# Optimization experiments

Measured on AMD Instinct MI355X. Metric: run time of the kernel, lower is better.

## Reference

```python
import jax, jax.numpy as jnp
import numpy as np

# Dimensions (see shape_source)
D = 12       # tree depth / number of levels
N = 32768    # nodes per level
L = 3        # label_size
K = 4        # nary (max children)
HID = 128    # hidden_size == dim_E == dim_rep
V = 50000    # word_vocab_size
LAYERS = 2   # stacked NaryTreeLSTM layers


def setup_inputs() -> dict:
    key = jax.random.key(0)
    ks = jax.random.split(key, 10)
    s = 0.02  # weight init scale
    tokens = jax.random.randint(ks[0], (D, N, L), 0, V)
    # child indices in [-1, N]; -1 = no child, 0 = zero init row, 1..N = prev-level node
    indices = jax.random.randint(ks[1], (D, N, K), 0, N + 2) - 1
    E = jax.random.normal(ks[2], (V, HID))  # torch.randn init
    lin_w = jax.random.normal(ks[3], (HID, L * HID)) * s
    lin_b = jnp.zeros((HID,), jnp.float32)
    Uf_w = jax.random.normal(ks[4], (LAYERS, K * HID, K * HID)) * s
    Uf_b = jnp.zeros((LAYERS, K * HID), jnp.float32)
    Uiuo_w = jax.random.normal(ks[5], (LAYERS, 3 * HID, K * HID)) * s
    Uiuo_b = jnp.zeros((LAYERS, 3 * HID), jnp.float32)
    W_w = jax.random.normal(ks[6], (LAYERS, 4 * HID, HID)) * s
    W_b = jnp.zeros((LAYERS, 4 * HID), jnp.float32)
    return dict(tokens=tokens, indices=indices, E=E, lin_w=lin_w, lin_b=lin_b,
                Uf_w=Uf_w, Uf_b=Uf_b, Uiuo_w=Uiuo_w, Uiuo_b=Uiuo_b, W_w=W_w, W_b=W_b)


def _tree_lstm_layer(x, indices, Uf_w, Uf_b, Uiuo_w, Uiuo_b, W_w, W_b):
    """x: [D,N,HID], indices: [D,N,K] in [-1,N]. Returns (hs, cs): [D,N,HID]."""
    d = HID

    def step(carry, inp):
        h_full, c_full = carry              # [1+N, d]; row 0 is the zero init state
        xl, idx = inp                       # [N, d], [N, K]
        mask = (idx != -1)
        safe = jnp.where(mask, idx, 0)
        h = h_full[safe]                    # [N, K, d] gather of child hidden states
        c = c_full[safe]                    # [N, K, d]
        m = mask.astype(xl.dtype)[..., None]
        Wx = xl @ W_w.T + W_b               # [N, 4d]
        Wf, Wi, Wu, Wo = Wx[:, :d], Wx[:, d:2 * d], Wx[:, 2 * d:3 * d], Wx[:, 3 * d:]
        h_flat = h.reshape(N, K * d)
        fk = jax.nn.sigmoid(Wf[:, None, :] + (h_flat @ Uf_w.T + Uf_b).reshape(N, K, d))
        f = jnp.sum(fk * c * m, axis=1)     # masked sum over children
        iuo = h_flat @ Uiuo_w.T + Uiuo_b    # [N, 3d]
        i = jax.nn.sigmoid(iuo[:, :d] + Wi)
        u = jnp.tanh(iuo[:, d:2 * d] + Wu)
        o = jax.nn.sigmoid(iuo[:, 2 * d:] + Wo)
        new_c = i * u + f
        new_h = o * jnp.tanh(new_c)
        zero = jnp.zeros((1, d), xl.dtype)
        new_carry = (jnp.concatenate([zero, new_h], 0), jnp.concatenate([zero, new_c], 0))
        return new_carry, (new_h, new_c)

    init = (jnp.zeros((1 + N, d), x.dtype), jnp.zeros((1 + N, d), x.dtype))
    _, (hs, cs) = jax.lax.scan(step, init, (x, indices))
    return hs, cs


def reference(tokens, indices, E, lin_w, lin_b, Uf_w, Uf_b, Uiuo_w, Uiuo_b, W_w, W_b):
    # TreeEmbeddingLayer: gather token embeddings, concat label slots, project to HID
    emb = E[tokens].reshape(D, N, L * HID) @ lin_w.T + lin_b  # [D, N, HID]
    t = emb
    cs = None
    for l in range(LAYERS):
        skip = t
        hs, cs = _tree_lstm_layer(t, indices, Uf_w[l], Uf_b[l], Uiuo_w[l], Uiuo_b[l], W_w[l], W_b[l])
        t = hs + skip  # residual over levels
    hx = jnp.tile(t[-1][None], (2, 1, 1))   # [2, N, HID]
    cx = jnp.tile(cs[-1][None], (2, 1, 1))  # [2, N, HID]
    return hx, cx
```

## Files before the change

kernel.cpp:

```cpp
#include <hip/hip_runtime.h>
#include <cstdint>
#include <cstddef>

#define DD 12
#define NNODE 32768
#define LTOK 3
#define KCH 4
#define HD 128
#define NC_STEP 896
#define KD_STEP 640
#define NC_EMB 128
#define KD_EMB 384

typedef unsigned short u16;
typedef __attribute__((ext_vector_type(8))) __bf16 bf16x8;
typedef __attribute__((ext_vector_type(4))) float f32x4;

__device__ __forceinline__ float bf2f(unsigned int u) {
  union { unsigned int i; float f; } v; v.i = (u & 0xffffu) << 16; return v.f;
}
__device__ __forceinline__ u16 f2bf(float f) {
  union { float f; unsigned int i; } v; v.f = f;
  unsigned int x = v.i;
  return (u16)((x + 0x7fffu + ((x >> 16) & 1u)) >> 16);
}
__device__ __forceinline__ float sigm(float x) { return 1.f / (1.f + __expf(-x)); }
__device__ __forceinline__ float tanh_fast(float x) { return 1.f - 2.f / (1.f + __expf(2.f * x)); }
__device__ __forceinline__ uint4 pack8(const float* p) {
  float4 a = *(const float4*)p;
  float4 b = *(const float4*)(p + 4);
  uint4 r;
  r.x = (unsigned)f2bf(a.x) | ((unsigned)f2bf(a.y) << 16);
  r.y = (unsigned)f2bf(a.z) | ((unsigned)f2bf(a.w) << 16);
  r.z = (unsigned)f2bf(b.x) | ((unsigned)f2bf(b.y) << 16);
  r.w = (unsigned)f2bf(b.z) | ((unsigned)f2bf(b.w) << 16);
  return r;
}
__device__ __forceinline__ void async16(const void* g, void* l) {
  __builtin_amdgcn_global_load_lds((const __attribute__((address_space(1))) unsigned int*)g,
                                   (__attribute__((address_space(3))) unsigned int*)l, 16, 0, 0);
}

template <int MODE, int NC, int KD>
__global__ __launch_bounds__(256) void gemm_k(
    const u16* __restrict__ Abf, const float* __restrict__ Tf,
    const int* __restrict__ gidx, const u16* __restrict__ B,
    const float* __restrict__ bias, u16* __restrict__ outb,
    float* __restrict__ outf, const u16* __restrict__ zbuf)
{
  __shared__ u16 As[128 * 64];
  __shared__ u16 Bs[128 * 64];
  const int t = threadIdx.x;
  const int w = t >> 6;
  const int L = t & 63;
  const int q = L >> 4;
  const int lrow8 = L >> 3;
  const int sub = L & 7;
  const int swz = sub ^ lrow8;
  const int row0 = blockIdx.x * 128;
  const int col0 = blockIdx.y * 128;

  f32x4 acc[4][4];
#pragma unroll
  for (int a = 0; a < 4; ++a)
#pragma unroll
    for (int b = 0; b < 4; ++b)
      acc[a][b] = f32x4{0.f, 0.f, 0.f, 0.f};

  const int mrow = (w & 1) * 64;
  const int ncol = (w >> 1) * 64;

  int4 cidx[4];
#pragma unroll
  for (int jj = 0; jj < 4; ++jj) {
    const int rit = w * 32 + jj * 8 + lrow8;
    if constexpr (MODE == 0) {
      cidx[jj] = *(const int4*)&gidx[(row0 + rit) * KCH];
    } else {
      cidx[jj].x = gidx[(row0 + rit) * LTOK + 0];
      cidx[jj].y = gidx[(row0 + rit) * LTOK + 1];
      cidx[jj].z = gidx[(row0 + rit) * LTOK + 2];
    }
  }

#pragma unroll
  for (int k0 = 0; k0 < KD; k0 += 64) {
    __syncthreads();
    if (MODE == 1 || k0 < 4 * HD) {
#pragma unroll
      for (int jj = 0; jj < 4; ++jj) {
        const int id = ((const int*)&cidx[jj])[k0 >> 7];
        const u16* base;
        if constexpr (MODE == 0)
          base = (id >= 1) ? (Abf + (size_t)(id - 1) * HD) : zbuf;
        else
          base = Abf + (size_t)id * HD;
        async16(base + (k0 & 127) + swz * 8, &As[(w * 32 + jj * 8) * 64]);
        const int rit = w * 32 + jj * 8 + lrow8;
        async16(B + (size_t)(col0 + rit) * KD + k0 + swz * 8, &Bs[(w * 32 + jj * 8) * 64]);
      }
    } else {
      uint4 va[4];
#pragma unroll
      for (int jj = 0; jj < 4; ++jj) {
        const int rit = w * 32 + jj * 8 + lrow8;
        va[jj] = pack8(Tf + (size_t)(row0 + rit) * HD + (k0 - 4 * HD) + swz * 8);
        async16(B + (size_t)(col0 + rit) * KD + k0 + swz * 8, &Bs[(w * 32 + jj * 8) * 64]);
      }
#pragma unroll
      for (int jj = 0; jj < 4; ++jj)
        *(uint4*)&As[(w * 32 + jj * 8 + lrow8) * 64 + sub * 8] = va[jj];
    }
    __syncthreads();
#pragma unroll
    for (int ks = 0; ks < 2; ++ks) {
      bf16x8 af[4], bfr[4];
      const int pc = ((ks * 4 + q) ^ (L & 7)) * 8;
#pragma unroll
      for (int mt = 0; mt < 4; ++mt)
        af[mt] = *(const bf16x8*)&As[(mrow + mt * 16 + (L & 15)) * 64 + pc];
#pragma unroll
      for (int nt = 0; nt < 4; ++nt)
        bfr[nt] = *(const bf16x8*)&Bs[(ncol + nt * 16 + (L & 15)) * 64 + pc];
#pragma unroll
      for (int mt = 0; mt < 4; ++mt)
#pragma unroll
        for (int nt = 0; nt < 4; ++nt)
          acc[mt][nt] = __builtin_amdgcn_mfma_f32_16x16x32_bf16(af[mt], bfr[nt], acc[mt][nt], 0, 0, 0);
    }
  }

#pragma unroll
  for (int nt = 0; nt < 4; ++nt) {
    const int col = col0 + ncol + nt * 16 + (L & 15);
    const float bb = bias[col];
#pragma unroll
    for (int mt = 0; mt < 4; ++mt) {
#pragma unroll
      for (int i = 0; i < 4; ++i) {
        const int row = row0 + mrow + mt * 16 + q * 4 + i;
        const float v = acc[mt][nt][i] + bb;
        if constexpr (MODE == 1) outf[(size_t)row * NC + col] = v;
        else                     outb[(size_t)row * NC + col] = f2bf(v);
      }
    }
  }
}

__global__ __launch_bounds__(256) void cell_k(
    const u16* __restrict__ pre, const int* __restrict__ idxs,
    const float* __restrict__ c_prev, float* __restrict__ c_cur,
    u16* __restrict__ h_cur, float* __restrict__ t_io)
{
  const int g = blockIdx.x * 256 + threadIdx.x;
  const int r = g >> 7;
  const int j = g & 127;
  const u16* pr = pre + (size_t)r * NC_STEP;
  float f = 0.f;
#pragma unroll
  for (int k = 0; k < KCH; ++k) {
    const int id = idxs[r * KCH + k];
    const float cg = (id >= 1) ? c_prev[(size_t)(id - 1) * HD + j] : 0.f;
    f += sigm(bf2f(pr[k * HD + j])) * cg;
  }
  const float iv = sigm(bf2f(pr[4 * HD + j]));
  const float uv = tanh_fast(bf2f(pr[5 * HD + j]));
  const float ov = sigm(bf2f(pr[6 * HD + j]));
  const float cn = iv * uv + f;
  const float hv = ov * tanh_fast(cn);
  c_cur[g] = cn;
  h_cur[g] = f2bf(hv);
  t_io[g] = t_io[g] + hv;
}

__global__ __launch_bounds__(256) void conv_k(const float* __restrict__ src,
                                              u16* __restrict__ dst, int n4)
{
  const int g = blockIdx.x * 256 + threadIdx.x;
  if (g < n4) {
    float4 v = ((const float4*)src)[g];
    ((ushort4*)dst)[g] = make_ushort4(f2bf(v.x), f2bf(v.y), f2bf(v.z), f2bf(v.w));
  }
}

__global__ __launch_bounds__(256) void prep_k(
    const float* __restrict__ Uf_w, const float* __restrict__ Uf_b,
    const float* __restrict__ Uiuo_w, const float* __restrict__ Uiuo_b,
    const float* __restrict__ W_w, const float* __restrict__ W_b,
    u16* __restrict__ Ubig, float* __restrict__ biasbig)
{
  const int l = blockIdx.y;
  const int e = blockIdx.x * 256 + threadIdx.x;
  const int c = e / KD_STEP;
  const int k = e % KD_STEP;
  float v;
  if (k < 512) {
    v = (c < 512) ? Uf_w[((size_t)l * 512 + c) * 512 + k]
                  : Uiuo_w[((size_t)l * 384 + (c - 512)) * 512 + k];
  } else {
    const int q = k - 512;
    const int wr = (c < 512) ? (c & 127) : (128 + (c - 512));
    v = W_w[((size_t)l * 512 + wr) * 128 + q];
  }
  Ubig[((size_t)l * 896 + c) * 640 + k] = f2bf(v);
  if (e < 896) {
    const float b = (e < 512)
        ? (Uf_b[l * 512 + e] + W_b[l * 512 + (e & 127)])
        : (Uiuo_b[l * 384 + (e - 512)] + W_b[l * 512 + 128 + (e - 512)]);
    biasbig[l * 896 + e] = b;
  }
}

__global__ __launch_bounds__(256) void fin_k(
    const float* __restrict__ t_fin, const float* __restrict__ c_fin,
    float* __restrict__ out)
{
  const size_t NH = (size_t)NNODE * HD;
  const size_t g = (size_t)blockIdx.x * 256 + threadIdx.x;
  const float h = t_fin[g];
  const float c = c_fin[g];
  out[g] = h;
  out[NH + g] = h;
  out[2 * NH + g] = c;
  out[3 * NH + g] = c;
}

extern "C" void kernel_launch(void* const* d_in, const int* in_sizes, int n_in,
                              void* d_out, int out_size, void* d_ws, size_t ws_size,
                              hipStream_t stream)
{
  (void)in_sizes; (void)n_in; (void)out_size; (void)ws_size;
  const int*   tokens  = (const int*)d_in[0];
  const int*   indices = (const int*)d_in[1];
  const float* E       = (const float*)d_in[2];
  const float* lin_w   = (const float*)d_in[3];
  const float* lin_b   = (const float*)d_in[4];
  const float* Uf_w    = (const float*)d_in[5];
  const float* Uf_b    = (const float*)d_in[6];
  const float* Uiuo_w  = (const float*)d_in[7];
  const float* Uiuo_b  = (const float*)d_in[8];
  const float* W_w     = (const float*)d_in[9];
  const float* W_b     = (const float*)d_in[10];
  float* out = (float*)d_out;

  const size_t NH = (size_t)NNODE * HD;

  char* ws = (char*)d_ws;
  size_t off = 0;
  auto alloc = [&](size_t bytes) -> void* {
    void* p = ws + off;
    off = (off + bytes + 255) & ~(size_t)255;
    return p;
  };
  u16*   Ubig    = (u16*)alloc((size_t)2 * 896 * 640 * 2);
  float* biasbig = (float*)alloc(2 * 896 * 4);
  u16*   Ebf     = (u16*)alloc((size_t)50000 * HD * 2);
  u16*   Lbf     = (u16*)alloc((size_t)HD * KD_EMB * 2);
  float* tslice  = (float*)alloc(NH * 4);
  u16*   h0a     = (u16*)alloc(NH * 2);
  u16*   h0b     = (u16*)alloc(NH * 2);
  u16*   h1a     = (u16*)alloc(NH * 2);
  u16*   h1b     = (u16*)alloc(NH * 2);
  float* c0a     = (float*)alloc(NH * 4);
  float* c0b     = (float*)alloc(NH * 4);
  float* c1a     = (float*)alloc(NH * 4);
  float* c1b     = (float*)alloc(NH * 4);
  u16*   pre     = (u16*)alloc((size_t)NNODE * NC_STEP * 2);
  u16*   zbuf    = (u16*)alloc(512);

  u16*   h0[2] = {h0a, h0b};
  u16*   h1[2] = {h1a, h1b};
  float* c0[2] = {c0a, c0b};
  float* c1[2] = {c1a, c1b};

  hipMemsetAsync(zbuf, 0, 512, stream);
  hipMemsetAsync(h0[0], 0, NH * 2, stream);
  hipMemsetAsync(h1[0], 0, NH * 2, stream);
  hipMemsetAsync(c0[0], 0, NH * 4, stream);
  hipMemsetAsync(c1[0], 0, NH * 4, stream);
  prep_k<<<dim3(2240, 2), 256, 0, stream>>>(Uf_w, Uf_b, Uiuo_w, Uiuo_b, W_w, W_b,
                                            Ubig, biasbig);
  conv_k<<<dim3((50000 * HD / 4 + 255) / 256), 256, 0, stream>>>(E, Ebf, 50000 * HD / 4);
  conv_k<<<dim3((HD * KD_EMB / 4 + 255) / 256), 256, 0, stream>>>(lin_w, Lbf, HD * KD_EMB / 4);

  for (int d = 0; d < DD; ++d) {
    const int ri = d & 1, wi = (d + 1) & 1;
    const int* idxd = indices + (size_t)d * NNODE * KCH;
    const int* tokd = tokens + (size_t)d * NNODE * LTOK;

    gemm_k<1, NC_EMB, KD_EMB><<<dim3(NNODE / 128, 1), 256, 0, stream>>>(
        Ebf, nullptr, tokd, Lbf, lin_b, nullptr, tslice, zbuf);

    for (int l = 0; l < 2; ++l) {
      const u16*   hp = (l == 0) ? h0[ri] : h1[ri];
      u16*         hc = (l == 0) ? h0[wi] : h1[wi];
      const float* cp = (l == 0) ? c0[ri] : c1[ri];
      float*       cc = (l == 0) ? c0[wi] : c1[wi];
      const u16* Ul = Ubig + (size_t)l * 896 * 640;
      const float* bl = biasbig + l * 896;
      gemm_k<0, NC_STEP, KD_STEP><<<dim3(NNODE / 128, NC_STEP / 128), 256, 0, stream>>>(
          hp, tslice, idxd, Ul, bl, pre, nullptr, zbuf);
      cell_k<<<dim3((int)(NH / 256)), 256, 0, stream>>>(
          pre, idxd, cp, cc, hc, tslice);
    }
  }
  fin_k<<<dim3((int)(NH / 256)), 256, 0, stream>>>(tslice, c1[0], out);
}
```

Before: 2.364 ms.

## Rewrite step GEMM as 256x128 double-buffered 8-wave kernel with bf16 residual copy

Replaces the per-step gated GEMM with a 512-thread kernel using 256x128 tiles, double-buffered LDS with async global-to-LDS loads interleaved across MFMA phases, s_setprio around the MFMAs, and an XCD-aware block remap. The embedding and cell kernels now also write a bf16 copy of the residual stream, so the GEMM can async-load the x operand instead of converting fp32 to bf16 in registers. The aim is to hide load latency and cut conversion work in the dominant GEMM, at the cost of an extra bf16 buffer write per cell and more LDS per block.

```diff
diff --git a/kernel.cpp b/kernel.cpp
--- a/kernel.cpp
+++ b/kernel.cpp
@@ -26,27 +26,148 @@
 }
 __device__ __forceinline__ float sigm(float x) { return 1.f / (1.f + __expf(-x)); }
 __device__ __forceinline__ float tanh_fast(float x) { return 1.f - 2.f / (1.f + __expf(2.f * x)); }
-__device__ __forceinline__ uint4 pack8(const float* p) {
-  float4 a = *(const float4*)p;
-  float4 b = *(const float4*)(p + 4);
-  uint4 r;
-  r.x = (unsigned)f2bf(a.x) | ((unsigned)f2bf(a.y) << 16);
-  r.y = (unsigned)f2bf(a.z) | ((unsigned)f2bf(a.w) << 16);
-  r.z = (unsigned)f2bf(b.x) | ((unsigned)f2bf(b.y) << 16);
-  r.w = (unsigned)f2bf(b.z) | ((unsigned)f2bf(b.w) << 16);
-  return r;
-}
 __device__ __forceinline__ void async16(const void* g, void* l) {
   __builtin_amdgcn_global_load_lds((const __attribute__((address_space(1))) unsigned int*)g,
                                    (__attribute__((address_space(3))) unsigned int*)l, 16, 0, 0);
 }
 
-template <int MODE, int NC, int KD>
-__global__ __launch_bounds__(256) void gemm_k(
-    const u16* __restrict__ Abf, const float* __restrict__ Tf,
+#define BM 256
+#define BN 128
+#define BK 64
+
+__global__ __launch_bounds__(512) void gemm8_k(
+    const u16* __restrict__ Abf, const u16* __restrict__ Tbf,
     const int* __restrict__ gidx, const u16* __restrict__ B,
     const float* __restrict__ bias, u16* __restrict__ outb,
-    float* __restrict__ outf, const u16* __restrict__ zbuf)
+    const u16* __restrict__ zbuf)
+{
+  __shared__ u16 As[2][BM * BK];
+  __shared__ u16 Bs[2][BN * BK];
+  const int t = threadIdx.x;
+  const int w = t >> 6;
+  const int L = t & 63;
+  const int q = L >> 4;
+  const int lrow8 = L >> 3;
+  const int sub = L & 7;
+  const int swz = sub ^ lrow8;
+
+  const int bid = blockIdx.x;
+  const int wg = (bid & 7) * 112 + (bid >> 3);
+  const int rt = wg / 7;
+  const int ct = wg - rt * 7;
+  const int row0 = rt * BM;
+  const int col0 = ct * BN;
+
+  const int wm = w >> 2;
+  const int wn = w & 3;
+  const int mrow = wm * 128;
+  const int ncol = wn * 32;
+
+  f32x4 acc[8][2];
+#pragma unroll
+  for (int a = 0; a < 8; ++a)
+#pragma unroll
+    for (int b = 0; b < 2; ++b)
+      acc[a][b] = f32x4{0.f, 0.f, 0.f, 0.f};
+
+  int4 cidx[4];
+#pragma unroll
+  for (int jj = 0; jj < 4; ++jj)
+    cidx[jj] = *(const int4*)&gidx[(row0 + w * 32 + jj * 8 + lrow8) * KCH];
+
+  auto stageB = [&](const int k0, const int sel, const int jb) {
+    const int r = w * 16 + jb * 8;
+    async16(B + (size_t)(col0 + r + lrow8) * KD_STEP + k0 + swz * 8,
+            &Bs[sel][r * BK]);
+  };
+  auto stageA = [&](const int k0, const int sel, const int jj) {
+    const int rbase = w * 32 + jj * 8;
+    const u16* src;
+    if (k0 < 4 * HD) {
+      const int id = ((const int*)&cidx[jj])[k0 >> 7];
+      const u16* base = (id >= 1) ? (Abf + (size_t)(id - 1) * HD) : zbuf;
+      src = base + (k0 & 127) + swz * 8;
+    } else {
+      src = Tbf + (size_t)(row0 + rbase + lrow8) * HD + (k0 - 4 * HD) + swz * 8;
+    }
+    async16(src, &As[sel][rbase * BK]);
+  };
+
+  stageB(0, 0, 0); stageB(0, 0, 1);
+  stageA(0, 0, 0); stageA(0, 0, 1); stageA(0, 0, 2); stageA(0, 0, 3);
+  asm volatile("s_waitcnt vmcnt(0)" ::: "memory");
+  __builtin_amdgcn_s_barrier();
+
+  constexpr int NT = KD_STEP / BK;
+  bf16x8 bf[2][2];
+#pragma unroll
+  for (int tt = 0; tt < NT; ++tt) {
+    const int rd = tt & 1, wr = (tt + 1) & 1;
+    const int k1 = (tt + 1) * BK;
+#pragma unroll
+    for (int p = 0; p < 4; ++p) {
+      if (p == 0) {
+#pragma unroll
+        for (int nt = 0; nt < 2; ++nt)
+#pragma unroll
+          for (int ks = 0; ks < 2; ++ks)
+            bf[nt][ks] = *(const bf16x8*)&Bs[rd][(ncol + nt * 16 + (L & 15)) * BK +
+                                                 (((ks * 4 + q) ^ (L & 7)) * 8)];
+      }
+      bf16x8 af[2][2];
+#pragma unroll
+      for (int half = 0; half < 2; ++half)
+#pragma unroll
+        for (int ks = 0; ks < 2; ++ks)
+          af[half][ks] = *(const bf16x8*)&As[rd][(mrow + (p + half * 4) * 16 + (L & 15)) * BK +
+                                                 (((ks * 4 + q) ^ (L & 7)) * 8)];
+      if (tt + 1 < NT) {
+        if (p == 0)      { stageB(k1, wr, 0); stageB(k1, wr, 1); }
+        else if (p == 1) { stageA(k1, wr, 0); stageA(k1, wr, 1); }
+        else if (p == 2) { stageA(k1, wr, 2); stageA(k1, wr, 3); }
+      }
+      __builtin_amdgcn_s_barrier();
+      asm volatile("s_waitcnt lgkmcnt(0)" ::: "memory");
+      __builtin_amdgcn_sched_barrier(0);
+      __builtin_amdgcn_s_setprio(1);
+#pragma unroll
+      for (int half = 0; half < 2; ++half)
+#pragma unroll
+        for (int nt = 0; nt < 2; ++nt)
+#pragma unroll
+          for (int ks = 0; ks < 2; ++ks)
+            acc[p + half * 4][nt] = __builtin_amdgcn_mfma_f32_16x16x32_bf16(
+                af[half][ks], bf[nt][ks], acc[p + half * 4][nt], 0, 0, 0);
+      __builtin_amdgcn_s_setprio(0);
+      __builtin_amdgcn_sched_barrier(0);
+      if (p == 0) {
+        if (tt + 1 < NT) asm volatile("s_waitcnt vmcnt(2)" ::: "memory");
+        else             asm volatile("s_waitcnt vmcnt(0)" ::: "memory");
+      }
+      if (p == 3 && tt + 1 < NT) asm volatile("s_waitcnt vmcnt(2)" ::: "memory");
+      __builtin_amdgcn_s_barrier();
+    }
+  }
+
+#pragma unroll
+  for (int nt = 0; nt < 2; ++nt) {
+    const int col = col0 + ncol + nt * 16 + (L & 15);
+    const float bb = bias[col];
+#pragma unroll
+    for (int mt = 0; mt < 8; ++mt) {
+#pragma unroll
+      for (int i = 0; i < 4; ++i) {
+        const int row = row0 + mrow + mt * 16 + q * 4 + i;
+        outb[(size_t)row * NC_STEP + col] = f2bf(acc[mt][nt][i] + bb);
+      }
+    }
+  }
+}
+
+__global__ __launch_bounds__(256) void gemm_emb_k(
+    const u16* __restrict__ Ebf, const int* __restrict__ tokd,
+    const u16* __restrict__ Lbf, const float* __restrict__ bias,
+    float* __restrict__ outf, u16* __restrict__ outb)
 {
   __shared__ u16 As[128 * 64];
   __shared__ u16 Bs[128 * 64];
@@ -58,7 +179,6 @@
   const int sub = L & 7;
   const int swz = sub ^ lrow8;
   const int row0 = blockIdx.x * 128;
-  const int col0 = blockIdx.y * 128;
 
   f32x4 acc[4][4];
 #pragma unroll
@@ -74,42 +194,22 @@
 #pragma unroll
   for (int jj = 0; jj < 4; ++jj) {
     const int rit = w * 32 + jj * 8 + lrow8;
-    if constexpr (MODE == 0) {
-      cidx[jj] = *(const int4*)&gidx[(row0 + rit) * KCH];
-    } else {
-      cidx[jj].x = gidx[(row0 + rit) * LTOK + 0];
-      cidx[jj].y = gidx[(row0 + rit) * LTOK + 1];
-      cidx[jj].z = gidx[(row0 + rit) * LTOK + 2];
-    }
-  }
-
-#pragma unroll
-  for (int k0 = 0; k0 < KD; k0 += 64) {
+    cidx[jj].x = tokd[(row0 + rit) * LTOK + 0];
+    cidx[jj].y = tokd[(row0 + rit) * LTOK + 1];
+    cidx[jj].z = tokd[(row0 + rit) * LTOK + 2];
+    cidx[jj].w = 0;
+  }
+
+#pragma unroll
+  for (int k0 = 0; k0 < KD_EMB; k0 += 64) {
     __syncthreads();
-    if (MODE == 1 || k0 < 4 * HD) {
-#pragma unroll
-      for (int jj = 0; jj < 4; ++jj) {
-        const int id = ((const int*)&cidx[jj])[k0 >> 7];
-        const u16* base;
-        if constexpr (MODE == 0)
-          base = (id >= 1) ? (Abf + (size_t)(id - 1) * HD) : zbuf;
-        else
-          base = Abf + (size_t)id * HD;
-        async16(base + (k0 & 127) + swz * 8, &As[(w * 32 + jj * 8) * 64]);
-        const int rit = w * 32 + jj * 8 + lrow8;
-        async16(B + (size_t)(col0 + rit) * KD + k0 + swz * 8, &Bs[(w * 32 + jj * 8) * 64]);
-      }
-    } else {
-      uint4 va[4];
-#pragma unroll
-      for (int jj = 0; jj < 4; ++jj) {
-        const int rit = w * 32 + jj * 8 + lrow8;
-        va[jj] = pack8(Tf + (size_t)(row0 + rit) * HD + (k0 - 4 * HD) + swz * 8);
-        async16(B + (size_t)(col0 + rit) * KD + k0 + swz * 8, &Bs[(w * 32 + jj * 8) * 64]);
-      }
-#pragma unroll
-      for (int jj = 0; jj < 4; ++jj)
-        *(uint4*)&As[(w * 32 + jj * 8 + lrow8) * 64 + sub * 8] = va[jj];
+#pragma unroll
+    for (int jj = 0; jj < 4; ++jj) {
+      const int id = ((const int*)&cidx[jj])[k0 >> 7];
+      const u16* base = Ebf + (size_t)id * HD;
+      const int rit = w * 32 + jj * 8 + lrow8;
+      async16(base + (k0 & 127) + swz * 8, &As[(w * 32 + jj * 8) * 64]);
+      async16(Lbf + (size_t)rit * KD_EMB + k0 + swz * 8, &Bs[(w * 32 + jj * 8) * 64]);
     }
     __syncthreads();
 #pragma unroll
@@ -132,7 +232,7 @@
 
 #pragma unroll
   for (int nt = 0; nt < 4; ++nt) {
-    const int col = col0 + ncol + nt * 16 + (L & 15);
+    const int col = ncol + nt * 16 + (L & 15);
     const float bb = bias[col];
 #pragma unroll
     for (int mt = 0; mt < 4; ++mt) {
@@ -140,8 +240,8 @@
       for (int i = 0; i < 4; ++i) {
         const int row = row0 + mrow + mt * 16 + q * 4 + i;
         const float v = acc[mt][nt][i] + bb;
-        if constexpr (MODE == 1) outf[(size_t)row * NC + col] = v;
-        else                     outb[(size_t)row * NC + col] = f2bf(v);
+        outf[(size_t)row * NC_EMB + col] = v;
+        outb[(size_t)row * NC_EMB + col] = f2bf(v);
       }
     }
   }
@@ -150,7 +250,7 @@
 __global__ __launch_bounds__(256) void cell_k(
     const u16* __restrict__ pre, const int* __restrict__ idxs,
     const float* __restrict__ c_prev, float* __restrict__ c_cur,
-    u16* __restrict__ h_cur, float* __restrict__ t_io)
+    u16* __restrict__ h_cur, float* __restrict__ t_io, u16* __restrict__ tbf)
 {
   const int g = blockIdx.x * 256 + threadIdx.x;
   const int r = g >> 7;
@@ -170,7 +270,9 @@
   const float hv = ov * tanh_fast(cn);
   c_cur[g] = cn;
   h_cur[g] = f2bf(hv);
-  t_io[g] = t_io[g] + hv;
+  const float tn = t_io[g] + hv;
+  t_io[g] = tn;
+  tbf[g] = f2bf(tn);
 }
 
 __global__ __launch_bounds__(256) void conv_k(const float* __restrict__ src,
@@ -257,6 +359,7 @@
   u16*   Ebf     = (u16*)alloc((size_t)50000 * HD * 2);
   u16*   Lbf     = (u16*)alloc((size_t)HD * KD_EMB * 2);
   float* tslice  = (float*)alloc(NH * 4);
+  u16*   tbf     = (u16*)alloc(NH * 2);
   u16*   h0a     = (u16*)alloc(NH * 2);
   u16*   h0b     = (u16*)alloc(NH * 2);
   u16*   h1a     = (u16*)alloc(NH * 2);
@@ -288,8 +391,8 @@
     const int* idxd = indices + (size_t)d * NNODE * KCH;
     const int* tokd = tokens + (size_t)d * NNODE * LTOK;
 
-    gemm_k<1, NC_EMB, KD_EMB><<<dim3(NNODE / 128, 1), 256, 0, stream>>>(
-        Ebf, nullptr, tokd, Lbf, lin_b, nullptr, tslice, zbuf);
+    gemm_emb_k<<<dim3(NNODE / 128), 256, 0, stream>>>(
+        Ebf, tokd, Lbf, lin_b, tslice, tbf);
 
     for (int l = 0; l < 2; ++l) {
       const u16*   hp = (l == 0) ? h0[ri] : h1[ri];
@@ -298,10 +401,10 @@
       float*       cc = (l == 0) ? c0[wi] : c1[wi];
       const u16* Ul = Ubig + (size_t)l * 896 * 640;
       const float* bl = biasbig + l * 896;
-      gemm_k<0, NC_STEP, KD_STEP><<<dim3(NNODE / 128, NC_STEP / 128), 256, 0, stream>>>(
-          hp, tslice, idxd, Ul, bl, pre, nullptr, zbuf);
+      gemm8_k<<<dim3((NNODE / BM) * (NC_STEP / BN)), 512, 0, stream>>>(
+          hp, tbf, idxd, Ul, bl, pre, zbuf);
       cell_k<<<dim3((int)(NH / 256)), 256, 0, stream>>>(
-          pre, idxd, cp, cc, hc, tslice);
+          pre, idxd, cp, cc, hc, tslice, tbf);
     }
   }
   fin_k<<<dim3((int)(NH / 256)), 256, 0, stream>>>(tslice, c1[0], out);
```

Result: slower. 2.632 ms (+11.3%).
